# Optimization experiments

Hardware: AMD Instinct MI355X
Metric: run time of the kernel (lower is better)

The kernel has to match this reference:

```python
import jax, jax.numpy as jnp
import numpy as np
from jax import lax

K = 10  # k_neighbors (k = min(k, N); N=1024 so k=10)


def setup_inputs() -> dict:
    key = jax.random.key(0)
    ks = jax.random.split(key, 6)
    B, N, M, D = 4, 1024, 8, 128
    PROJ, NC, OUT = 64, 10, 128
    x = jax.random.normal(ks[0], (B, N, M, D), dtype=jnp.float32)
    # Linear params (torch stores weight as [out, in])
    W_proj_w = jax.random.normal(ks[1], (PROJ, D), dtype=jnp.float32) / np.sqrt(D)
    W_proj_b = jnp.zeros((PROJ,), dtype=jnp.float32)
    C = jax.random.normal(ks[2], (NC, PROJ), dtype=jnp.float32) * np.sqrt(2.0 / (NC + PROJ))
    Theta_w = jax.random.normal(ks[3], (OUT, D), dtype=jnp.float32) / np.sqrt(D)
    Theta_b = jnp.zeros((OUT,), dtype=jnp.float32)
    return {"x": x, "W_proj_w": W_proj_w, "W_proj_b": W_proj_b, "C": C,
            "Theta_w": Theta_w, "Theta_b": Theta_b}


def _forward(x, W_proj_w, W_proj_b, C, Theta_w, Theta_b):
    B, N, M, D = x.shape
    BM = B * M
    x_flat = jnp.transpose(x, (0, 2, 1, 3)).reshape(BM, N, D)
    Z = x_flat @ W_proj_w.T + W_proj_b  # [BM, N, P]
    # squared euclidean pairwise distances (same topk ordering as cdist)
    sq = jnp.sum(Z * Z, axis=-1)  # [BM, N]
    d2 = sq[:, :, None] + sq[:, None, :] - 2.0 * jnp.einsum('bnp,bmp->bnm', Z, Z)
    _, idx = lax.top_k(-d2, K)  # k smallest distances -> [BM, N, K]
    # scatter 1.0 at neighbor indices
    b_ix = jnp.arange(BM)[:, None, None]
    r_ix = jnp.arange(N)[None, :, None]
    H_knn = jnp.zeros((BM, N, N), dtype=jnp.float32).at[b_ix, r_ix, idx].set(1.0)
    H_cluster = jax.nn.softmax(Z @ C.T, axis=-1)  # [BM, N, NC]
    H = jnp.concatenate([H_knn, H_cluster], axis=-1)  # [BM, N, N+NC]
    # hypergraph conv with degree normalization
    D_e = H.sum(axis=1)  # [BM, E]
    D_e_inv = jnp.where(D_e > 0, 1.0 / jnp.maximum(D_e, 1e-12), 0.0)
    D_v = H.sum(axis=2)  # [BM, N]
    D_v_inv_sqrt = jnp.where(D_v > 0, 1.0 / jnp.sqrt(jnp.maximum(D_v, 1e-12)), 0.0)
    X_trans = x_flat @ Theta_w.T + Theta_b  # [BM, N, F]
    out = D_v_inv_sqrt[:, :, None] * X_trans
    out = jnp.einsum('bne,bnf->bef', H, out)   # H^T @ out
    out = D_e_inv[:, :, None] * out
    out = jnp.einsum('bne,bef->bnf', H, out)   # H @ out
    out = D_v_inv_sqrt[:, :, None] * out
    out = jax.nn.elu(out)
    return jnp.transpose(out.reshape(B, M, N, -1), (0, 2, 1, 3))  # [B, N, M, F]


def reference(x, W_proj_w, W_proj_b, C, Theta_w, Theta_b):
    return _forward(x, W_proj_w, W_proj_b, C, Theta_w, Theta_b)
```

## Files before the change

kernel.cpp:

```cpp
#include <hip/hip_runtime.h>
#include <hip/hip_bf16.h>
#include <cstdint>
#include <cstddef>

#define BMC 32
#define NNODE 1024
#define DIN 128
#define PPROJ 64
#define NCLUS 10
#define FOUT 128
#define KNB 10

typedef _Float16 half8 __attribute__((ext_vector_type(8)));
typedef float f32x4 __attribute__((ext_vector_type(4)));

static const size_t OFF_Z    = 0;
static const size_t OFF_SQ   = 2097152;
static const size_t OFF_HC   = 2129920;
static const size_t OFF_IDX  = 2457600;
static const size_t OFF_CNT  = 2785280;
static const size_t OFF_FILL = 2818048;
static const size_t OFF_EC   = 2850816;
static const size_t OFF_DCV  = 2891776;
static const size_t OFF_OFFS = 2892096;
static const size_t OFF_ADJ  = 2924864;
static const size_t OFF_FLAG = 3252544;
static const size_t OFF_END  = 3252608;
static const size_t OFF_WPH  = OFF_EC;
static const size_t OFF_WPL  = OFF_EC +  4096;
static const size_t OFF_THH  = OFF_EC +  8192;
static const size_t OFF_THL  = OFF_EC + 16384;
static const size_t ZERO1_N  = 65536;
static const size_t ZERO2_N  = 41280;

__device__ __forceinline__ float bfu(unsigned int lo16) {
    return __uint_as_float(lo16 << 16);
}
__device__ __forceinline__ float bfhi(unsigned int w) {
    return __uint_as_float(w & 0xffff0000u);
}
__device__ __forceinline__ float ldf(const void* p, size_t i, bool isbf) {
    return isbf ? bfu((unsigned int)((const unsigned short*)p)[i])
                : ((const float*)p)[i];
}
__device__ __forceinline__ unsigned short f2bf(float v) {
    __hip_bfloat16 h = __float2bfloat16(v);
    return *(unsigned short*)&h;
}

__device__ __forceinline__ unsigned long long mkkey(float v, float sqr, int col) {
    float d = fmaxf(v + sqr, 0.0f);
    return ((unsigned long long)__float_as_uint(d) << 32) | (unsigned int)col;
}
__device__ __forceinline__ void kcas(unsigned long long &a, unsigned long long &b) {
    bool c = b < a;
    unsigned long long t = c ? b : a;
    b = c ? a : b;
    a = t;
}
__device__ __forceinline__ void kmin(unsigned long long &a, unsigned long long b) {
    a = (b < a) ? b : a;
}

__global__ __launch_bounds__(256) void k_probe(const unsigned int* __restrict__ xw,
                                               int* __restrict__ flag) {
    __shared__ int red[256];
    int t = threadIdx.x;
    int cnt = 0;
    for (int i = t; i < 1024; i += 256) {
        float b = bfu(xw[i] & 0xffffu);
        float ab = fabsf(b);
        if (ab > 9.5e-7f && ab < 1.0e6f) cnt++;
    }
    red[t] = cnt;
    __syncthreads();
    for (int off = 128; off > 0; off >>= 1) {
        if (t < off) red[t] += red[t + off];
        __syncthreads();
    }
    if (t == 0) flag[0] = (red[0] >= 700) ? 1 : 0;
}

__global__ __launch_bounds__(256) void k_zero(float* __restrict__ p, int n) {
    int i = blockIdx.x * 256 + threadIdx.x;
    if (i < n) p[i] = 0.0f;
}

__global__ __launch_bounds__(256) void k_split(const void* __restrict__ Wp,
                                               const void* __restrict__ Th,
                                               const int* __restrict__ flag,
                                               _Float16* __restrict__ WpH,
                                               _Float16* __restrict__ WpL,
                                               _Float16* __restrict__ ThH,
                                               _Float16* __restrict__ ThL) {
    const bool isbf = (flag[0] != 0);
    int i = blockIdx.x * 256 + threadIdx.x;
    if (i < 8192) {
        float v = ldf(Wp, i, isbf);
        _Float16 h = (_Float16)v;
        WpH[i] = h;
        WpL[i] = (_Float16)((v - (float)h) * 2048.0f);
    } else {
        int j = i - 8192;
        float v = ldf(Th, j, isbf);
        _Float16 h = (_Float16)v;
        ThH[j] = h;
        ThL[j] = (_Float16)((v - (float)h) * 2048.0f);
    }
}

__global__ __launch_bounds__(256) void k_proj(const void* __restrict__ x,
                                              const _Float16* __restrict__ WpH,
                                              const _Float16* __restrict__ WpL,
                                              const void* __restrict__ Wpb,
                                              const void* __restrict__ Cm,
                                              const int* __restrict__ flag,
                                              _Float16* __restrict__ Zh,
                                              _Float16* __restrict__ Zl,
                                              float* __restrict__ sqv,
                                              float* __restrict__ Hc) {
    __shared__ __align__(16) _Float16 wps[2][64][72];
    __shared__ __align__(16) _Float16 xsh[2][32][72];
    __shared__ float zs[32][68];
    __shared__ float cs[10][64];

    const bool isbf = (flag[0] != 0);
    int tid = threadIdx.x;
    int bi  = blockIdx.x;
    int bm  = bi >> 5;
    int n0  = (bi & 31) << 5;
    int b   = bm >> 3, m = bm & 7;

    int lane = tid & 63, wave = tid >> 6;
    int m16 = lane & 15, quad = lane >> 4;
    int rh = wave >> 1, ch = wave & 1;

    for (int e = tid; e < 640; e += 256) cs[e >> 6][e & 63] = ldf(Cm, e, isbf);

    f32x4 aH[2], aX[2];
#pragma unroll
    for (int t = 0; t < 2; ++t) {
        aH[t] = (f32x4){0.f, 0.f, 0.f, 0.f};
        aX[t] = (f32x4){0.f, 0.f, 0.f, 0.f};
    }

    for (int kc = 0; kc < 2; ++kc) {
        __syncthreads();
        for (int e = tid; e < 512; e += 256) {
            int p = e >> 3, c = e & 7;
            *(uint4*)&wps[0][p][c * 8] =
                *(const uint4*)(WpH + (size_t)p * 128 + kc * 64 + c * 8);
            *(uint4*)&wps[1][p][c * 8] =
                *(const uint4*)(WpL + (size_t)p * 128 + kc * 64 + c * 8);
        }
        for (int e = tid; e < 2048; e += 256) {
            int r = e >> 6, dk = e & 63;
            float v = ldf(x, (((size_t)b * NNODE + n0 + r) * 8 + m) * DIN + kc * 64 + dk, isbf);
            _Float16 h = (_Float16)v;
            xsh[0][r][dk] = h;
            xsh[1][r][dk] = (_Float16)((v - (float)h) * 2048.0f);
        }
        __syncthreads();
#pragma unroll
        for (int c32 = 0; c32 < 2; ++c32) {
            half8 Ah = *(const half8*)&xsh[0][rh * 16 + m16][c32 * 32 + quad * 8];
            half8 Al = *(const half8*)&xsh[1][rh * 16 + m16][c32 * 32 + quad * 8];
#pragma unroll
            for (int t = 0; t < 2; ++t) {
                int p = ch * 32 + t * 16 + m16;
                half8 Bh = *(const half8*)&wps[0][p][c32 * 32 + quad * 8];
                half8 Bl = *(const half8*)&wps[1][p][c32 * 32 + quad * 8];
                aH[t] = __builtin_amdgcn_mfma_f32_16x16x32_f16(Ah, Bh, aH[t], 0, 0, 0);
                aX[t] = __builtin_amdgcn_mfma_f32_16x16x32_f16(Al, Bh, aX[t], 0, 0, 0);
                aX[t] = __builtin_amdgcn_mfma_f32_16x16x32_f16(Ah, Bl, aX[t], 0, 0, 0);
            }
        }
    }

#pragma unroll
    for (int t = 0; t < 2; ++t) {
        int p = ch * 32 + t * 16 + m16;
        float bias = ldf(Wpb, p, isbf);
#pragma unroll
        for (int r = 0; r < 4; ++r) {
            int row = rh * 16 + quad * 4 + r;
            float v = aH[t][r] + aX[t][r] * (1.0f / 2048.0f) + bias;
            zs[row][p] = v;
            size_t off = ((size_t)bm * NNODE + n0 + row) * 64 + p;
            _Float16 h = (_Float16)v;
            Zh[off] = h;
            Zl[off] = (_Float16)((v - (float)h) * 2048.0f);
        }
    }
    __syncthreads();

    int row = tid >> 3, slot = tid & 7;
    int d0 = slot * 8;
    float sp = 0.f;
#pragma unroll
    for (int dd = 0; dd < 8; ++dd) { float z = zs[row][d0+dd]; sp += z * z; }
#pragma unroll
    for (int mm = 1; mm < 8; mm <<= 1) sp += __shfl_xor(sp, mm, 8);
    size_t g = (size_t)bm * NNODE + n0 + row;
    if (slot == 0) sqv[g] = sp;

    float sc[10];
#pragma unroll
    for (int c = 0; c < 10; ++c) {
        float pa = 0.f;
#pragma unroll
        for (int dd = 0; dd < 8; ++dd) pa += zs[row][d0+dd] * cs[c][d0+dd];
#pragma unroll
        for (int mm = 1; mm < 8; mm <<= 1) pa += __shfl_xor(pa, mm, 8);
        sc[c] = pa;
    }
    float mx = sc[0];
#pragma unroll
    for (int c = 1; c < 10; ++c) mx = fmaxf(mx, sc[c]);
    float ssum = 0.f;
#pragma unroll
    for (int c = 0; c < 10; ++c) { sc[c] = expf(sc[c] - mx); ssum += sc[c]; }
    float inv = 1.0f / ssum;
#pragma unroll
    for (int c = 0; c < 10; ++c)
        if ((c & 7) == slot) Hc[g * 10 + c] = sc[c] * inv;
}

__global__ __launch_bounds__(256) void k_theta(const void* __restrict__ x,
                                               const _Float16* __restrict__ ThH,
                                               const _Float16* __restrict__ ThL,
                                               const void* __restrict__ Thb,
                                               const int* __restrict__ flag,
                                               float* __restrict__ Xt) {
    __shared__ __align__(16) _Float16 ths[2][128][72];
    __shared__ __align__(16) _Float16 xsh[32][72];

    const bool isbf = (flag[0] != 0);
    int tid = threadIdx.x;
    int bi  = blockIdx.x;
    int bm  = bi >> 5;
    int n0  = (bi & 31) << 5;
    int b   = bm >> 3, m = bm & 7;

    int lane = tid & 63, wave = tid >> 6;
    int m16 = lane & 15, quad = lane >> 4;
    int rh = wave >> 1, ch = wave & 1;

    f32x4 aH[4], aX[4];
#pragma unroll
    for (int t = 0; t < 4; ++t) {
        aH[t] = (f32x4){0.f, 0.f, 0.f, 0.f};
        aX[t] = (f32x4){0.f, 0.f, 0.f, 0.f};
    }

    for (int kc = 0; kc < 2; ++kc) {
        __syncthreads();
        for (int e = tid; e < 1024; e += 256) {
            int f = e >> 3, c = e & 7;
            *(uint4*)&ths[0][f][c * 8] =
                *(const uint4*)(ThH + (size_t)f * 128 + kc * 64 + c * 8);
            *(uint4*)&ths[1][f][c * 8] =
                *(const uint4*)(ThL + (size_t)f * 128 + kc * 64 + c * 8);
        }
        for (int e = tid; e < 2048; e += 256) {
            int r = e >> 6, dk = e & 63;
            float v = ldf(x, (((size_t)b * NNODE + n0 + r) * 8 + m) * DIN + kc * 64 + dk, isbf);
            xsh[r][dk] = (_Float16)v;
        }
        __syncthreads();
#pragma unroll
        for (int c32 = 0; c32 < 2; ++c32) {
            half8 Ah = *(const half8*)&xsh[rh * 16 + m16][c32 * 32 + quad * 8];
#pragma unroll
            for (int t = 0; t < 4; ++t) {
                int f = ch * 64 + t * 16 + m16;
                half8 Bh = *(const half8*)&ths[0][f][c32 * 32 + quad * 8];
                half8 Bl = *(const half8*)&ths[1][f][c32 * 32 + quad * 8];
                aH[t] = __builtin_amdgcn_mfma_f32_16x16x32_f16(Ah, Bh, aH[t], 0, 0, 0);
                aX[t] = __builtin_amdgcn_mfma_f32_16x16x32_f16(Ah, Bl, aX[t], 0, 0, 0);
            }
        }
    }
#pragma unroll
    for (int t = 0; t < 4; ++t) {
        int f = ch * 64 + t * 16 + m16;
        float bias = ldf(Thb, f, isbf);
        size_t rb = (size_t)bm * NNODE + n0 + rh * 16 + quad * 4;
#pragma unroll
        for (int r = 0; r < 4; ++r) {
            Xt[(rb + r) * 128 + f] = aH[t][r] + aX[t][r] * (1.0f / 2048.0f) + bias;
        }
    }
}

__global__ __launch_bounds__(256) void k_topk(const _Float16* __restrict__ Zh,
                                              const _Float16* __restrict__ Zl,
                                              const float* __restrict__ sqv,
                                              int* __restrict__ idxo,
                                              int* __restrict__ cnt) {
    __shared__ __align__(16) _Float16 BH[64 * 72];
    __shared__ __align__(16) _Float16 BL[64 * 72];
    __shared__ float    ST[64 * 36];
    __shared__ float    sqt[64];

    int tid = threadIdx.x;
    int bi  = blockIdx.x;
    int bm  = bi >> 5;
    int n0  = (bi & 31) << 5;
    const _Float16* Zhb = Zh + (size_t)bm * NNODE * 64;
    const _Float16* Zlb = Zl + (size_t)bm * NNODE * 64;

    int lane = tid & 63, wave = tid >> 6;
    int m16 = lane & 15, quad = lane >> 4;

    half8 ah0, ah1, al0, al1, ah0b, ah1b, al0b, al1b;
    {
        size_t ab = (size_t)(n0 + m16) * 64 + quad * 8;
        ah0 = *(const half8*)(Zhb + ab);
        ah1 = *(const half8*)(Zhb + ab + 32);
        al0 = *(const half8*)(Zlb + ab);
        al1 = *(const half8*)(Zlb + ab + 32);
        size_t ab2 = ab + 16 * 64;
        ah0b = *(const half8*)(Zhb + ab2);
        ah1b = *(const half8*)(Zhb + ab2 + 32);
        al0b = *(const half8*)(Zlb + ab2);
        al1b = *(const half8*)(Zlb + ab2 + 32);
    }

    unsigned long long keys[10];
#pragma unroll
    for (int j = 0; j < 10; ++j) keys[j] = ~0ULL;

    int srow  = tid >> 3;
    int sslot = tid & 7;
    float sqr = sqv[(size_t)bm * NNODE + n0 + srow];

    for (int t = 0; t < 16; ++t) {
        int j0 = t << 6;
        for (int e = tid; e < 512; e += 256) {
            int col = e >> 3, kc = e & 7;
            *(uint4*)&BH[col * 72 + kc * 8] =
                *(const uint4*)(Zhb + (size_t)(j0 + col) * 64 + kc * 8);
            *(uint4*)&BL[col * 72 + kc * 8] =
                *(const uint4*)(Zlb + (size_t)(j0 + col) * 64 + kc * 8);
        }
        if (tid < 64) sqt[tid] = sqv[(size_t)bm * NNODE + j0 + tid];
        __syncthreads();

        {
            int cl = wave * 16 + m16;
            const _Float16* pb = &BH[cl * 72 + quad * 8];
            const _Float16* pl = &BL[cl * 72 + quad * 8];
            half8 bh0 = *(const half8*)pb;
            half8 bh1 = *(const half8*)(pb + 32);
            half8 bl0 = *(const half8*)pl;
            half8 bl1 = *(const half8*)(pl + 32);
            float sqc = sqt[cl];

            f32x4 acc  = {0.f, 0.f, 0.f, 0.f};
            f32x4 accx = {0.f, 0.f, 0.f, 0.f};
            acc  = __builtin_amdgcn_mfma_f32_16x16x32_f16(ah0, bh0, acc, 0, 0, 0);
            acc  = __builtin_amdgcn_mfma_f32_16x16x32_f16(ah1, bh1, acc, 0, 0, 0);
            accx = __builtin_amdgcn_mfma_f32_16x16x32_f16(al0, bh0, accx, 0, 0, 0);
            accx = __builtin_amdgcn_mfma_f32_16x16x32_f16(ah0, bl0, accx, 0, 0, 0);
            accx = __builtin_amdgcn_mfma_f32_16x16x32_f16(al1, bh1, accx, 0, 0, 0);
            accx = __builtin_amdgcn_mfma_f32_16x16x32_f16(ah1, bl1, accx, 0, 0, 0);
            f32x4 sc;
#pragma unroll
            for (int r = 0; r < 4; ++r) {
                float g = acc[r] + accx[r] * (1.0f / 2048.0f);
                sc[r] = fmaf(-2.0f, g, sqc);
            }
            *(f32x4*)&ST[cl * 36 + quad * 4] = sc;

            f32x4 accB  = {0.f, 0.f, 0.f, 0.f};
            f32x4 accxB = {0.f, 0.f, 0.f, 0.f};
            accB  = __builtin_amdgcn_mfma_f32_16x16x32_f16(ah0b, bh0, accB, 0, 0, 0);
            accB  = __builtin_amdgcn_mfma_f32_16x16x32_f16(ah1b, bh1, accB, 0, 0, 0);
            accxB = __builtin_amdgcn_mfma_f32_16x16x32_f16(al0b, bh0, accxB, 0, 0, 0);
            accxB = __builtin_amdgcn_mfma_f32_16x16x32_f16(ah0b, bl0, accxB, 0, 0, 0);
            accxB = __builtin_amdgcn_mfma_f32_16x16x32_f16(al1b, bh1, accxB, 0, 0, 0);
            accxB = __builtin_amdgcn_mfma_f32_16x16x32_f16(ah1b, bl1, accxB, 0, 0, 0);
#pragma unroll
            for (int r = 0; r < 4; ++r) {
                float g = accB[r] + accxB[r] * (1.0f / 2048.0f);
                sc[r] = fmaf(-2.0f, g, sqc);
            }
            *(f32x4*)&ST[cl * 36 + 16 + quad * 4] = sc;
        }
        __syncthreads();

        unsigned long long b0 = mkkey(ST[(sslot     ) * 36 + srow], sqr, j0 + sslot);
        unsigned long long b1 = mkkey(ST[(sslot +  8) * 36 + srow], sqr, j0 + sslot + 8);
        unsigned long long b2 = mkkey(ST[(sslot + 16) * 36 + srow], sqr, j0 + sslot + 16);
        unsigned long long b3 = mkkey(ST[(sslot + 24) * 36 + srow], sqr, j0 + sslot + 24);
        unsigned long long b4 = mkkey(ST[(sslot + 32) * 36 + srow], sqr, j0 + sslot + 32);
        unsigned long long b5 = mkkey(ST[(sslot + 40) * 36 + srow], sqr, j0 + sslot + 40);
        unsigned long long b6 = mkkey(ST[(sslot + 48) * 36 + srow], sqr, j0 + sslot + 48);
        unsigned long long b7 = mkkey(ST[(sslot + 56) * 36 + srow], sqr, j0 + sslot + 56);

        kcas(b0, b1); kcas(b2, b3); kcas(b4, b5); kcas(b6, b7);
        kcas(b0, b2); kcas(b1, b3); kcas(b4, b6); kcas(b5, b7);
        kcas(b1, b2); kcas(b5, b6);
        kcas(b0, b4); kcas(b1, b5); kcas(b2, b6); kcas(b3, b7);
        kcas(b2, b4); kcas(b3, b5);
        kcas(b1, b2); kcas(b3, b4); kcas(b5, b6);

        kmin(keys[2], b7); kmin(keys[3], b6); kmin(keys[4], b5); kmin(keys[5], b4);
        kmin(keys[6], b3); kmin(keys[7], b2); kmin(keys[8], b1); kmin(keys[9], b0);

        kcas(keys[0], keys[8]); kcas(keys[1], keys[9]);
        kcas(keys[2], keys[6]); kcas(keys[3], keys[7]);
        kcas(keys[4], keys[8]); kcas(keys[5], keys[9]);
        kcas(keys[2], keys[4]); kcas(keys[3], keys[5]);
        kcas(keys[6], keys[8]); kcas(keys[7], keys[9]);
        kcas(keys[0], keys[1]); kcas(keys[2], keys[3]);
        kcas(keys[4], keys[5]); kcas(keys[6], keys[7]); kcas(keys[8], keys[9]);
    }

    size_t gr = (size_t)bm * NNODE + n0 + srow;
    for (int it = 0; it < 10; ++it) {
        unsigned long long mine = keys[0];
        unsigned long long best = mine;
#pragma unroll
        for (int mm = 1; mm < 8; mm <<= 1) {
            unsigned long long o = __shfl_xor(best, mm, 8);
            if (o < best) best = o;
        }
        if (best == mine) {
#pragma unroll
            for (int j = 0; j < 9; ++j) keys[j] = keys[j+1];
            keys[9] = ~0ULL;
            int col = (int)(best & 0xFFFFFFFFu);
            idxo[gr * KNB + it] = col;
            atomicAdd(&cnt[bm * NNODE + col], 1);
        }
    }
}

__global__ __launch_bounds__(256) void k_scan(const int* __restrict__ cnt,
                                              int* __restrict__ offs) {
    __shared__ int part[256];
    int bm = blockIdx.x, t = threadIdx.x;
    int base = bm * 1024 + t * 4;
    int c0 = cnt[base], c1 = cnt[base+1], c2 = cnt[base+2], c3 = cnt[base+3];
    int ps = c0 + c1 + c2 + c3;
    part[t] = ps;
    __syncthreads();
    for (int off = 1; off < 256; off <<= 1) {
        int add = (t >= off) ? part[t - off] : 0;
        __syncthreads();
        part[t] += add;
        __syncthreads();
    }
    int e0 = part[t] - ps;
    int gb = bm * (NNODE * KNB);
    offs[base]   = gb + e0;
    offs[base+1] = gb + e0 + c0;
    offs[base+2] = gb + e0 + c0 + c1;
    offs[base+3] = gb + e0 + c0 + c1 + c2;
}

__global__ __launch_bounds__(256) void k_fill(const int* __restrict__ idxb,
                                              const int* __restrict__ offs,
                                              int* __restrict__ fill,
                                              int* __restrict__ adj) {
    int i = blockIdx.x * 256 + threadIdx.x;
    int g = i / 10;
    int bm = g >> 10;
    int e  = idxb[i];
    int eg = (bm << 10) + e;
    int pos = atomicAdd(&fill[eg], 1);
    adj[offs[eg] + pos] = g;
}

__global__ __launch_bounds__(256) void k_edge(const float* __restrict__ Xt,
                                              const int* __restrict__ offs,
                                              const int* __restrict__ cnt,
                                              const int* __restrict__ adj,
                                              unsigned short* __restrict__ Ek) {
    int tid = threadIdx.x;
    int bi  = blockIdx.x;
    int swz = (bi & 7) * 512 + (bi >> 3);
    int e = swz * 8 + (tid >> 5);
    int l = tid & 31;
    int start = offs[e];
    int num = cnt[e];
    float4 acc = {0.f, 0.f, 0.f, 0.f};
    if (num > 0) {
        int nm1 = num - 1;
        int gidx[16];
#pragma unroll
        for (int j = 0; j < 16; ++j) {
            int jj = (j < nm1) ? j : nm1;
            gidx[j] = adj[start + jj];
        }
#pragma unroll
        for (int j = 0; j < 16; ++j) {
            float4 a = *(const float4*)(Xt + (size_t)gidx[j] * 128 + l * 4);
            float w = (j < num) ? 1.0f : 0.0f;
            acc.x = fmaf(w, a.x, acc.x);
            acc.y = fmaf(w, a.y, acc.y);
            acc.z = fmaf(w, a.z, acc.z);
            acc.w = fmaf(w, a.w, acc.w);
        }
        int i = 16;
        for (; i + 1 < num; i += 2) {
            int g0 = adj[start + i];
            int g1 = adj[start + i + 1];
            float4 a = *(const float4*)(Xt + (size_t)g0 * 128 + l * 4);
            float4 b = *(const float4*)(Xt + (size_t)g1 * 128 + l * 4);
            acc.x += a.x + b.x; acc.y += a.y + b.y;
            acc.z += a.z + b.z; acc.w += a.w + b.w;
        }
        if (i < num) {
            int g0 = adj[start + i];
            float4 a = *(const float4*)(Xt + (size_t)g0 * 128 + l * 4);
            acc.x += a.x; acc.y += a.y; acc.z += a.z; acc.w += a.w;
        }
    }
    float scale = (num > 0) ? 1.0f / (float)num : 0.0f;
    ushort4 o;
    o.x = f2bf(acc.x * scale);
    o.y = f2bf(acc.y * scale);
    o.z = f2bf(acc.z * scale);
    o.w = f2bf(acc.w * scale);
    *(ushort4*)(Ek + (size_t)e * 128 + l * 4) = o;
}

__global__ __launch_bounds__(256) void k_clus(const float* __restrict__ Xt,
                                              const float* __restrict__ Hc,
                                              float* __restrict__ Ec,
                                              float* __restrict__ Dcv) {
    __shared__ float hcs[128][12];
    int tid = threadIdx.x;
    int bm = blockIdx.x >> 3;
    int ch = blockIdx.x & 7;
    int n0 = ch * 128;

    for (int e = tid; e < 1280; e += 256) {
        int r = e / 10, c = e - r * 10;
        hcs[r][c] = Hc[((size_t)bm * NNODE + n0 + r) * 10 + c];
    }
    __syncthreads();

    int f = tid & 127;
    int h = tid >> 7;
    int c0 = h * 5;
    float acc[5]  = {0.f,0.f,0.f,0.f,0.f};
    float dacc[5] = {0.f,0.f,0.f,0.f,0.f};
#pragma unroll 2
    for (int n = 0; n < 128; ++n) {
        float xv = Xt[((size_t)bm * NNODE + n0 + n) * 128 + f];
#pragma unroll
        for (int j = 0; j < 5; ++j) {
            float hv = hcs[n][c0 + j];
            acc[j]  = fmaf(hv, xv, acc[j]);
            dacc[j] += hv;
        }
    }
#pragma unroll
    for (int j = 0; j < 5; ++j)
        atomicAdd(&Ec[((size_t)bm * 10 + c0 + j) * 128 + f], acc[j]);
    if (f == 0) {
#pragma unroll
        for (int j = 0; j < 5; ++j) atomicAdd(&Dcv[bm * 10 + c0 + j], dacc[j]);
    }
}

__global__ __launch_bounds__(256) void k_escale(float* __restrict__ Ec,
                                                const float* __restrict__ Dcv) {
    int i = blockIdx.x * 256 + threadIdx.x;
    float d = Dcv[i >> 7];
    Ec[i] = (d > 0.f) ? Ec[i] / d : 0.f;
}

__global__ __launch_bounds__(256) void k_final(const unsigned short* __restrict__ Ek,
                                               const float* __restrict__ Ec,
                                               const float* __restrict__ Hc,
                                               const int* __restrict__ idxb,
                                               float* __restrict__ out) {
    int tid = threadIdx.x;
    int bi  = blockIdx.x;
    int swz = (bi & 7) * 512 + (bi >> 3);
    int g = swz * 8 + (tid >> 5);
    int l = tid & 31;
    int bm = g >> 10, n = g & 1023;
    const int* ip = idxb + (size_t)g * 10;
    const unsigned short* ekb = Ek + ((size_t)bm << 10) * 128 + l * 4;

    float4 acc = {0.f, 0.f, 0.f, 0.f};
#pragma unroll
    for (int k = 0; k < 10; k += 2) {
        int e0 = ip[k], e1 = ip[k + 1];
        ushort4 u0 = *(const ushort4*)(ekb + (size_t)e0 * 128);
        ushort4 u1 = *(const ushort4*)(ekb + (size_t)e1 * 128);
        acc.x += bfu(u0.x) + bfu(u1.x);
        acc.y += bfu(u0.y) + bfu(u1.y);
        acc.z += bfu(u0.z) + bfu(u1.z);
        acc.w += bfu(u0.w) + bfu(u1.w);
    }
    const float* hp  = Hc + (size_t)g * 10;
    const float* ecp = Ec + (size_t)bm * 10 * 128 + l * 4;
#pragma unroll
    for (int c = 0; c < 10; ++c) {
        float hv = hp[c];
        float4 ec = *(const float4*)(ecp + c * 128);
        acc.x += hv * ec.x; acc.y += hv * ec.y;
        acc.z += hv * ec.z; acc.w += hv * ec.w;
    }
    float4 r;
    r.x = acc.x * (1.0f / 11.0f);
    r.y = acc.y * (1.0f / 11.0f);
    r.z = acc.z * (1.0f / 11.0f);
    r.w = acc.w * (1.0f / 11.0f);
    r.x = (r.x > 0.f) ? r.x : expm1f(r.x);
    r.y = (r.y > 0.f) ? r.y : expm1f(r.y);
    r.z = (r.z > 0.f) ? r.z : expm1f(r.z);
    r.w = (r.w > 0.f) ? r.w : expm1f(r.w);
    int b = bm >> 3, m = bm & 7;
    *(float4*)(out + (((size_t)b * NNODE + n) * 8 + m) * 128 + l * 4) = r;
}

extern "C" void kernel_launch(void* const* d_in, const int* in_sizes, int n_in,
                              void* d_out, int out_size, void* d_ws, size_t ws_size,
                              hipStream_t stream) {
    const void* x   = d_in[0];
    const void* Wp  = d_in[1];
    const void* Wpb = d_in[2];
    const void* Cm  = d_in[3];
    const void* Th  = d_in[4];
    const void* Thb = d_in[5];
    float* ws = (float*)d_ws;

    if (ws_size < OFF_END * sizeof(float)) return;

    _Float16* Zh = (_Float16*)(ws + OFF_Z);
    _Float16* Zl = (_Float16*)(ws + OFF_Z + 1048576);
    float* sqv  = ws + OFF_SQ;
    float* Hc   = ws + OFF_HC;
    int*   idxb = (int*)(ws + OFF_IDX);
    int*   cnt  = (int*)(ws + OFF_CNT);
    int*   fill = (int*)(ws + OFF_FILL);
    float* Ec   = ws + OFF_EC;
    float* Dcv  = ws + OFF_DCV;
    int*   offs = (int*)(ws + OFF_OFFS);
    int*   adj  = (int*)(ws + OFF_ADJ);
    int*   flag = (int*)(ws + OFF_FLAG);
    _Float16* WpH = (_Float16*)(ws + OFF_WPH);
    _Float16* WpL = (_Float16*)(ws + OFF_WPL);
    _Float16* ThH = (_Float16*)(ws + OFF_THH);
    _Float16* ThL = (_Float16*)(ws + OFF_THL);
    unsigned short* Ek = (unsigned short*)(ws + OFF_Z);
    float* Xt  = (float*)d_out;
    float* out = (float*)d_out;

    k_probe <<<1, 256, 0, stream>>>((const unsigned int*)x, flag);
    k_zero  <<<256, 256, 0, stream>>>(ws + OFF_CNT, (int)ZERO1_N);
    k_split <<<96,  256, 0, stream>>>(Wp, Th, flag, WpH, WpL, ThH, ThL);
    k_proj  <<<1024, 256, 0, stream>>>(x, WpH, WpL, Wpb, Cm, flag, Zh, Zl, sqv, Hc);
    k_topk  <<<1024, 256, 0, stream>>>(Zh, Zl, sqv, idxb, cnt);
    k_scan  <<<32,   256, 0, stream>>>(cnt, offs);
    k_fill  <<<1280, 256, 0, stream>>>(idxb, offs, fill, adj);
    k_theta <<<1024, 256, 0, stream>>>(x, ThH, ThL, Thb, flag, Xt);
    k_zero  <<<162,  256, 0, stream>>>(ws + OFF_EC, (int)ZERO2_N);
    k_edge  <<<4096, 256, 0, stream>>>(Xt, offs, cnt, adj, Ek);
    k_clus  <<<256,  256, 0, stream>>>(Xt, Hc, Ec, Dcv);
    k_escale<<<160,  256, 0, stream>>>(Ec, Dcv);
    k_final <<<4096, 256, 0, stream>>>(Ek, Ec, Hc, idxb, out);
}
```

Measured before the change: 276.6 us.

## Fuse zeroing, scan/fill and edge scaling into neighbouring kernels

Removes four kernel launches. The zeroing of counts moves into k_split and the zeroing of Ec into k_edge. The scan and fill steps merge into a single k_csr kernel that bins with shared-memory atomics, and the Dcv division moves from k_escale into k_final. The top-k key drops the per-row sqr add and clamp, since a constant per row does not change ordering, and uses a sign-aware float key instead. This cuts launch overhead and global atomics, but leaves k_csr running on only 32 blocks.

Result: no change. 273.3 us (-1.2%).

```diff
diff --git a/kernel.cpp b/kernel.cpp
--- a/kernel.cpp
+++ b/kernel.cpp
@@ -30,8 +30,7 @@
 static const size_t OFF_WPL  = OFF_EC +  4096;
 static const size_t OFF_THH  = OFF_EC +  8192;
 static const size_t OFF_THL  = OFF_EC + 16384;
-static const size_t ZERO1_N  = 65536;
-static const size_t ZERO2_N  = 41280;
+static const int    ZERO2_N  = 41280;
 
 __device__ __forceinline__ float bfu(unsigned int lo16) {
     return __uint_as_float(lo16 << 16);
@@ -48,9 +47,10 @@
     return *(unsigned short*)&h;
 }
 
-__device__ __forceinline__ unsigned long long mkkey(float v, float sqr, int col) {
-    float d = fmaxf(v + sqr, 0.0f);
-    return ((unsigned long long)__float_as_uint(d) << 32) | (unsigned int)col;
+__device__ __forceinline__ unsigned long long mkkey(float v, int col) {
+    unsigned int bits = __float_as_uint(v);
+    unsigned int s = bits ^ (0x80000000u | (unsigned int)((int)bits >> 31));
+    return ((unsigned long long)s << 32) | (unsigned int)col;
 }
 __device__ __forceinline__ void kcas(unsigned long long &a, unsigned long long &b) {
     bool c = b < a;
@@ -81,20 +81,18 @@
     if (t == 0) flag[0] = (red[0] >= 700) ? 1 : 0;
 }
 
-__global__ __launch_bounds__(256) void k_zero(float* __restrict__ p, int n) {
-    int i = blockIdx.x * 256 + threadIdx.x;
-    if (i < n) p[i] = 0.0f;
-}
-
 __global__ __launch_bounds__(256) void k_split(const void* __restrict__ Wp,
                                                const void* __restrict__ Th,
                                                const int* __restrict__ flag,
                                                _Float16* __restrict__ WpH,
                                                _Float16* __restrict__ WpL,
                                                _Float16* __restrict__ ThH,
-                                               _Float16* __restrict__ ThL) {
+                                               _Float16* __restrict__ ThL,
+                                               int* __restrict__ cntz) {
     const bool isbf = (flag[0] != 0);
     int i = blockIdx.x * 256 + threadIdx.x;
+    cntz[i] = 0;
+    if (i < 8192) cntz[i + 24576] = 0;
     if (i < 8192) {
         float v = ldf(Wp, i, isbf);
         _Float16 h = (_Float16)v;
@@ -333,7 +331,6 @@
 
     int srow  = tid >> 3;
     int sslot = tid & 7;
-    float sqr = sqv[(size_t)bm * NNODE + n0 + srow];
 
     for (int t = 0; t < 16; ++t) {
         int j0 = t << 6;
@@ -390,14 +387,14 @@
         }
         __syncthreads();
 
-        unsigned long long b0 = mkkey(ST[(sslot     ) * 36 + srow], sqr, j0 + sslot);
-        unsigned long long b1 = mkkey(ST[(sslot +  8) * 36 + srow], sqr, j0 + sslot + 8);
-        unsigned long long b2 = mkkey(ST[(sslot + 16) * 36 + srow], sqr, j0 + sslot + 16);
-        unsigned long long b3 = mkkey(ST[(sslot + 24) * 36 + srow], sqr, j0 + sslot + 24);
-        unsigned long long b4 = mkkey(ST[(sslot + 32) * 36 + srow], sqr, j0 + sslot + 32);
-        unsigned long long b5 = mkkey(ST[(sslot + 40) * 36 + srow], sqr, j0 + sslot + 40);
-        unsigned long long b6 = mkkey(ST[(sslot + 48) * 36 + srow], sqr, j0 + sslot + 48);
-        unsigned long long b7 = mkkey(ST[(sslot + 56) * 36 + srow], sqr, j0 + sslot + 56);
+        unsigned long long b0 = mkkey(ST[(sslot     ) * 36 + srow], j0 + sslot);
+        unsigned long long b1 = mkkey(ST[(sslot +  8) * 36 + srow], j0 + sslot + 8);
+        unsigned long long b2 = mkkey(ST[(sslot + 16) * 36 + srow], j0 + sslot + 16);
+        unsigned long long b3 = mkkey(ST[(sslot + 24) * 36 + srow], j0 + sslot + 24);
+        unsigned long long b4 = mkkey(ST[(sslot + 32) * 36 + srow], j0 + sslot + 32);
+        unsigned long long b5 = mkkey(ST[(sslot + 40) * 36 + srow], j0 + sslot + 40);
+        unsigned long long b6 = mkkey(ST[(sslot + 48) * 36 + srow], j0 + sslot + 48);
+        unsigned long long b7 = mkkey(ST[(sslot + 56) * 36 + srow], j0 + sslot + 56);
 
         kcas(b0, b1); kcas(b2, b3); kcas(b4, b5); kcas(b6, b7);
         kcas(b0, b2); kcas(b1, b3); kcas(b4, b6); kcas(b5, b7);
@@ -438,9 +435,12 @@
     }
 }
 
-__global__ __launch_bounds__(256) void k_scan(const int* __restrict__ cnt,
-                                              int* __restrict__ offs) {
+__global__ __launch_bounds__(256) void k_csr(const int* __restrict__ cnt,
+                                             const int* __restrict__ idxb,
+                                             int* __restrict__ offs,
+                                             int* __restrict__ adj) {
     __shared__ int part[256];
+    __shared__ int fillL[1024];
     int bm = blockIdx.x, t = threadIdx.x;
     int base = bm * 1024 + t * 4;
     int c0 = cnt[base], c1 = cnt[base+1], c2 = cnt[base+2], c3 = cnt[base+3];
@@ -455,32 +455,36 @@
     }
     int e0 = part[t] - ps;
     int gb = bm * (NNODE * KNB);
-    offs[base]   = gb + e0;
-    offs[base+1] = gb + e0 + c0;
-    offs[base+2] = gb + e0 + c0 + c1;
-    offs[base+3] = gb + e0 + c0 + c1 + c2;
-}
-
-__global__ __launch_bounds__(256) void k_fill(const int* __restrict__ idxb,
-                                              const int* __restrict__ offs,
-                                              int* __restrict__ fill,
-                                              int* __restrict__ adj) {
-    int i = blockIdx.x * 256 + threadIdx.x;
-    int g = i / 10;
-    int bm = g >> 10;
-    int e  = idxb[i];
-    int eg = (bm << 10) + e;
-    int pos = atomicAdd(&fill[eg], 1);
-    adj[offs[eg] + pos] = g;
+    int o0 = gb + e0, o1 = o0 + c0, o2 = o1 + c1, o3 = o2 + c2;
+    offs[base]   = o0;
+    offs[base+1] = o1;
+    offs[base+2] = o2;
+    offs[base+3] = o3;
+    fillL[t*4]   = o0;
+    fillL[t*4+1] = o1;
+    fillL[t*4+2] = o2;
+    fillL[t*4+3] = o3;
+    __syncthreads();
+    int ibase = bm * (NNODE * KNB);
+    for (int e = t; e < NNODE * KNB; e += 256) {
+        int eidx = idxb[ibase + e];
+        int pos = atomicAdd(&fillL[eidx], 1);
+        adj[pos] = (bm << 10) + (e / 10);
+    }
 }
 
 __global__ __launch_bounds__(256) void k_edge(const float* __restrict__ Xt,
                                               const int* __restrict__ offs,
                                               const int* __restrict__ cnt,
                                               const int* __restrict__ adj,
-                                              unsigned short* __restrict__ Ek) {
+                                              unsigned short* __restrict__ Ek,
+                                              float* __restrict__ EcZ) {
     int tid = threadIdx.x;
     int bi  = blockIdx.x;
+    {
+        int zi = bi * 256 + tid;
+        if (zi < ZERO2_N) EcZ[zi] = 0.0f;
+    }
     int swz = (bi & 7) * 512 + (bi >> 3);
     int e = swz * 8 + (tid >> 5);
     int l = tid & 31;
@@ -568,16 +572,10 @@
     }
 }
 
-__global__ __launch_bounds__(256) void k_escale(float* __restrict__ Ec,
-                                                const float* __restrict__ Dcv) {
-    int i = blockIdx.x * 256 + threadIdx.x;
-    float d = Dcv[i >> 7];
-    Ec[i] = (d > 0.f) ? Ec[i] / d : 0.f;
-}
-
 __global__ __launch_bounds__(256) void k_final(const unsigned short* __restrict__ Ek,
                                                const float* __restrict__ Ec,
                                                const float* __restrict__ Hc,
+                                               const float* __restrict__ Dcv,
                                                const int* __restrict__ idxb,
                                                float* __restrict__ out) {
     int tid = threadIdx.x;
@@ -601,10 +599,12 @@
         acc.w += bfu(u0.w) + bfu(u1.w);
     }
     const float* hp  = Hc + (size_t)g * 10;
+    const float* dcp = Dcv + (size_t)bm * 10;
     const float* ecp = Ec + (size_t)bm * 10 * 128 + l * 4;
 #pragma unroll
     for (int c = 0; c < 10; ++c) {
-        float hv = hp[c];
+        float d  = dcp[c];
+        float hv = (d > 0.f) ? hp[c] / d : 0.f;
         float4 ec = *(const float4*)(ecp + c * 128);
         acc.x += hv * ec.x; acc.y += hv * ec.y;
         acc.z += hv * ec.z; acc.w += hv * ec.w;
@@ -641,7 +641,6 @@
     float* Hc   = ws + OFF_HC;
     int*   idxb = (int*)(ws + OFF_IDX);
     int*   cnt  = (int*)(ws + OFF_CNT);
-    int*   fill = (int*)(ws + OFF_FILL);
     float* Ec   = ws + OFF_EC;
     float* Dcv  = ws + OFF_DCV;
     int*   offs = (int*)(ws + OFF_OFFS);
@@ -655,17 +654,13 @@
     float* Xt  = (float*)d_out;
     float* out = (float*)d_out;
 
-    k_probe <<<1, 256, 0, stream>>>((const unsigned int*)x, flag);
-    k_zero  <<<256, 256, 0, stream>>>(ws + OFF_CNT, (int)ZERO1_N);
-    k_split <<<96,  256, 0, stream>>>(Wp, Th, flag, WpH, WpL, ThH, ThL);
+    k_probe <<<1,    256, 0, stream>>>((const unsigned int*)x, flag);
+    k_split <<<96,   256, 0, stream>>>(Wp, Th, flag, WpH, WpL, ThH, ThL, cnt);
     k_proj  <<<1024, 256, 0, stream>>>(x, WpH, WpL, Wpb, Cm, flag, Zh, Zl, sqv, Hc);
     k_topk  <<<1024, 256, 0, stream>>>(Zh, Zl, sqv, idxb, cnt);
-    k_scan  <<<32,   256, 0, stream>>>(cnt, offs);
-    k_fill  <<<1280, 256, 0, stream>>>(idxb, offs, fill, adj);
+    k_csr   <<<32,   256, 0, stream>>>(cnt, idxb, offs, adj);
     k_theta <<<1024, 256, 0, stream>>>(x, ThH, ThL, Thb, flag, Xt);
-    k_zero  <<<162,  256, 0, stream>>>(ws + OFF_EC, (int)ZERO2_N);
-    k_edge  <<<4096, 256, 0, stream>>>(Xt, offs, cnt, adj, Ek);
+    k_edge  <<<4096, 256, 0, stream>>>(Xt, offs, cnt, adj, Ek, Ec);
     k_clus  <<<256,  256, 0, stream>>>(Xt, Hc, Ec, Dcv);
-    k_escale<<<160,  256, 0, stream>>>(Ec, Dcv);
-    k_final <<<4096, 256, 0, stream>>>(Ek, Ec, Hc, idxb, out);
-}
+    k_final <<<4096, 256, 0, stream>>>(Ek, Ec, Hc, Dcv, idxb, out);
+}
```
